# Kernel optimization log

Hardware: AMD Instinct MI355X
Metric: run time of the kernel (lower is better)

Reference implementation:

```python
import jax, jax.numpy as jnp
import numpy as np

SEQ = 110          # input_size1 = sample_width*2
HALF = SEQ // 2    # 55
N_EMBD = 102       # n_chrom + 2
HEAD = 192

def _cross_half_mask():
    # attention allowed only between the two halves (same-half blocks masked)
    idx = jnp.arange(SEQ)
    same_half = (idx[:, None] < HALF) == (idx[None, :] < HALF)
    return same_half  # True where attention is DISALLOWED

def setup_inputs() -> dict:
    key = jax.random.key(0)
    k1, k2, k3, k4 = jax.random.split(key, 4)
    B = 8192
    x = jax.random.normal(k1, (B, SEQ, N_EMBD), dtype=jnp.float32)
    Wq = jax.random.normal(k2, (N_EMBD, HEAD), dtype=jnp.float32) * (N_EMBD ** -0.5)
    Wk = jax.random.normal(k3, (N_EMBD, HEAD), dtype=jnp.float32) * (N_EMBD ** -0.5)
    Wv = jax.random.normal(k4, (N_EMBD, HEAD), dtype=jnp.float32) * (N_EMBD ** -0.5)
    return {"x": x, "Wq": Wq, "Wk": Wk, "Wv": Wv}

def reference(x, Wq, Wk, Wv):
    # q,k,v: [B, S, H]
    q = x @ Wq
    k = x @ Wk
    v = x @ Wv
    scale = HEAD ** -0.5
    scores = jnp.einsum('bsh,bth->bst', q, k) * scale  # [B, S, S]
    mask = _cross_half_mask()                           # [S, S] True = masked
    scores = jnp.where(mask, -jnp.inf, scores)
    attn = jax.nn.softmax(scores, axis=-1)
    # dropout is identity at inference (p=0.15 at train)
    out = jnp.einsum('bst,bth->bsh', attn, v)           # [B, S, H]
    return out
```

## Files before the change

kernel.cpp:

```cpp
#include <hip/hip_runtime.h>
#include <hip/hip_bf16.h>

#define SEQ   110
#define HALFS 55
#define EMB   102
#define HEAD  192

typedef short bf16x8 __attribute__((ext_vector_type(8)));
typedef float f32x4  __attribute__((ext_vector_type(4)));

#define XS    104
#define XTILE (64 * XS)
#define PS    72
#define MTS   128
#define MTROWS 112
#define MT_SHORTS (MTROWS * MTS)
#define WES   128

__device__ __forceinline__ short f2bf(float f) {
    unsigned u = __float_as_uint(f);
    unsigned r = u + 0x7fffu + ((u >> 16) & 1u);
    return (short)(r >> 16);
}
__device__ __forceinline__ unsigned pk2(float a, float b) {
    return ((unsigned)(unsigned short)f2bf(b) << 16) | (unsigned short)f2bf(a);
}

__global__ void prep(const float* __restrict__ Wq, const float* __restrict__ Wk,
                     const float* __restrict__ Wv, short* __restrict__ ws) {
    int flat = blockIdx.x * 256 + threadIdx.x;
    if (flat < MT_SHORTS) {
        int i = flat >> 7, j = flat & 127;
        float v = 0.0f;
        if (i < EMB && j < EMB) {
            const float4* q4 = (const float4*)(Wq + j * HEAD);
            const float4* k4 = (const float4*)(Wk + i * HEAD);
            float s = 0.0f;
            #pragma unroll 4
            for (int h4 = 0; h4 < HEAD / 4; ++h4) {
                float4 a = q4[h4], b = k4[h4];
                s += a.x * b.x + a.y * b.y + a.z * b.z + a.w * b.w;
            }
            v = s * 0.07216878364870322f;
        }
        ws[flat] = f2bf(v);
    } else if (flat < MT_SHORTS + HEAD * WES) {
        int idx = flat - MT_SHORTS;
        int h = idx >> 7, e = idx & 127;
        float v = (e < EMB) ? Wv[e * HEAD + h] : 0.0f;
        ws[flat] = f2bf(v);
    }
}

__global__ __launch_bounds__(512, 2)
void attn_head(const float* __restrict__ x, const short* __restrict__ ws,
               float* __restrict__ out, int B) {
    const int tid  = threadIdx.x;
    const int w8   = tid >> 6;
    const int h    = w8 >> 2;
    const int w4   = w8 & 3;
    const int lane = tid & 63;
    const int g    = lane >> 4;
    const int r    = lane & 15;

    __shared__ __attribute__((aligned(16))) short u[4 * XTILE];
    __shared__ __attribute__((aligned(16))) short P_lds[2][64 * PS];

    short* xh = u + h * XTILE;
    short* xo = u + (h ^ 1) * XTILE;
    short* yh = u + (2 + h) * XTILE;
    short* Ph = P_lds[h];

    const short* Mt  = ws;
    const short* WvT = ws + MT_SHORTS;

    bf16x8 wvf[3][4];
    #pragma unroll
    for (int mi = 0; mi < 3; ++mi) {
        const int hrow = 16 * (w4 + 4 * mi) + r;
        #pragma unroll
        for (int kk = 0; kk < 4; ++kk)
            wvf[mi][kk] = *(const bf16x8*)(WvT + hrow * WES + 32 * kk + 8 * g);
    }

    {
        unsigned long long* z = (unsigned long long*)u;
        if (tid < 468) z[(tid < 234 ? 1430 : 2860) + tid] = 0ull;
        if (tid < 110)
            *(unsigned*)(u + (tid & 1) * XTILE + (tid >> 1) * XS + 102) = 0u;
    }

    unsigned xv[11];
    auto loadx = [&](int batch) {
        const float2* xb2 = (const float2*)(x + (size_t)batch * (SEQ * EMB));
        #pragma unroll
        for (int it = 0; it < 11; ++it) {
            int idx = tid + it * 512;
            if (idx < 5610) { float2 v = xb2[idx]; xv[it] = pk2(v.x, v.y); }
        }
    };
    auto stagex = [&]() {
        #pragma unroll
        for (int it = 0; it < 11; ++it) {
            int idx = tid + it * 512;
            if (idx < 5610) {
                int row  = (int)(((unsigned)idx * 82242u) >> 22);
                int ec   = idx - 51 * row;
                int tile = row >= HALFS;
                int lr   = row - HALFS * tile;
                *(unsigned*)(u + tile * XTILE + lr * XS + 2 * ec) = xv[it];
            }
        }
    };

    loadx(blockIdx.x);
    const int stride = (int)gridDim.x;

    bf16x8 ax[4][4];
    bf16x8 zz = {};
    const int src0 = ((g & 1) << 5) + r;
    const int src1 = src0 + 16;
    const bool hi  = (g >> 1) != 0;

    #pragma unroll 1
    for (int p = blockIdx.x; p < B; p += stride) {
        stagex();
        __syncthreads();

        bf16x8 am[2][4];
        #pragma unroll
        for (int mi2 = 0; mi2 < 2; ++mi2) {
            const int mt = w4 + 4 * mi2;
            #pragma unroll
            for (int kk = 0; kk < 4; ++kk)
                am[mi2][kk] = (mt < 7) ? *(const bf16x8*)(Mt + (16 * mt + r) * MTS + 32 * kk + 8 * g) : zz;
        }

        #pragma unroll
        for (int stl = 0; stl < 4; ++stl) {
            const short* xb = xh + (16 * stl + r) * XS;
            bf16x8 bx[4];
            #pragma unroll
            for (int kk = 0; kk < 3; ++kk) bx[kk] = *(const bf16x8*)(xb + 32 * kk + 8 * g);
            bx[3] = zz;
            if (g == 0) bx[3] = *(const bf16x8*)(xb + 96);
            #pragma unroll
            for (int mi2 = 0; mi2 < 2; ++mi2) {
                const int mt = w4 + 4 * mi2;
                if (mt < 7) {
                    f32x4 acc = {0.f, 0.f, 0.f, 0.f};
                    #pragma unroll
                    for (int kk = 0; kk < 4; ++kk)
                        acc = __builtin_amdgcn_mfma_f32_16x16x32_bf16(am[mi2][kk], bx[kk], acc, 0, 0, 0);
                    if (mt < 6 || g < 2) {
                        uint2 t2; t2.x = pk2(acc[0], acc[1]); t2.y = pk2(acc[2], acc[3]);
                        *(uint2*)(yh + (16 * stl + r) * XS + 16 * mt + 4 * g) = t2;
                    }
                }
            }
        }

        #pragma unroll
        for (int mt = 0; mt < 4; ++mt) {
            const short* xb = xo + (16 * mt + r) * XS;
            #pragma unroll
            for (int kk = 0; kk < 3; ++kk) ax[mt][kk] = *(const bf16x8*)(xb + 32 * kk + 8 * g);
            ax[mt][3] = zz;
            if (g == 0) ax[mt][3] = *(const bf16x8*)(xb + 96);
        }

        unsigned vpk[4][3][2];
        #pragma unroll
        for (int st = 0; st < 4; ++st) {
            #pragma unroll
            for (int mi = 0; mi < 3; ++mi) {
                f32x4 acc = {0.f, 0.f, 0.f, 0.f};
                #pragma unroll
                for (int kk = 0; kk < 4; ++kk)
                    acc = __builtin_amdgcn_mfma_f32_16x16x32_bf16(ax[st][kk], wvf[mi][kk], acc, 0, 0, 0);
                vpk[st][mi][0] = pk2(acc[0], acc[1]);
                vpk[st][mi][1] = pk2(acc[2], acc[3]);
            }
        }
        bf16x8 va[3][2];
        #pragma unroll
        for (int mi = 0; mi < 3; ++mi) {
            unsigned e00 = (unsigned)__shfl((int)vpk[0][mi][0], src0), e01 = (unsigned)__shfl((int)vpk[0][mi][1], src0);
            unsigned e02 = (unsigned)__shfl((int)vpk[0][mi][0], src1), e03 = (unsigned)__shfl((int)vpk[0][mi][1], src1);
            unsigned f00 = (unsigned)__shfl((int)vpk[1][mi][0], src0), f01 = (unsigned)__shfl((int)vpk[1][mi][1], src0);
            unsigned f02 = (unsigned)__shfl((int)vpk[1][mi][0], src1), f03 = (unsigned)__shfl((int)vpk[1][mi][1], src1);
            uint4 u0;
            u0.x = hi ? f00 : e00; u0.y = hi ? f01 : e01; u0.z = hi ? f02 : e02; u0.w = hi ? f03 : e03;
            unsigned e10 = (unsigned)__shfl((int)vpk[2][mi][0], src0), e11 = (unsigned)__shfl((int)vpk[2][mi][1], src0);
            unsigned e12 = (unsigned)__shfl((int)vpk[2][mi][0], src1), e13 = (unsigned)__shfl((int)vpk[2][mi][1], src1);
            unsigned f10 = (unsigned)__shfl((int)vpk[3][mi][0], src0), f11 = (unsigned)__shfl((int)vpk[3][mi][1], src0);
            unsigned f12 = (unsigned)__shfl((int)vpk[3][mi][0], src1), f13 = (unsigned)__shfl((int)vpk[3][mi][1], src1);
            uint4 u1;
            u1.x = hi ? f10 : e10; u1.y = hi ? f11 : e11; u1.z = hi ? f12 : e12; u1.w = hi ? f13 : e13;
            __builtin_memcpy(&va[mi][0], &u0, 16);
            __builtin_memcpy(&va[mi][1], &u1, 16);
        }

        __syncthreads();

        if (p + stride < B) loadx(p + stride);

        {
            const short* yb = yh + (16 * w4 + r) * XS;
            bf16x8 by[4];
            #pragma unroll
            for (int kk = 0; kk < 3; ++kk) by[kk] = *(const bf16x8*)(yb + 32 * kk + 8 * g);
            by[3] = zz;
            if (g == 0) by[3] = *(const bf16x8*)(yb + 96);

            float sc[4][4];
            #pragma unroll
            for (int mt = 0; mt < 4; ++mt) {
                f32x4 acc = {0.f, 0.f, 0.f, 0.f};
                #pragma unroll
                for (int kk = 0; kk < 4; ++kk)
                    acc = __builtin_amdgcn_mfma_f32_16x16x32_bf16(ax[mt][kk], by[kk], acc, 0, 0, 0);
                #pragma unroll
                for (int j = 0; j < 4; ++j) sc[mt][j] = acc[j];
            }
            #pragma unroll
            for (int j = 0; j < 4; ++j)
                if (48 + 4 * g + j >= HALFS) sc[3][j] = -1e30f;

            float mx = -1e30f;
            #pragma unroll
            for (int mt = 0; mt < 4; ++mt) {
                #pragma unroll
                for (int j = 0; j < 4; ++j) mx = fmaxf(mx, sc[mt][j]);
            }
            mx = fmaxf(mx, __shfl_xor(mx, 16));
            mx = fmaxf(mx, __shfl_xor(mx, 32));
            float pr[4][4];
            float sum = 0.f;
            #pragma unroll
            for (int mt = 0; mt < 4; ++mt) {
                #pragma unroll
                for (int j = 0; j < 4; ++j) { pr[mt][j] = __expf(sc[mt][j] - mx); sum += pr[mt][j]; }
            }
            sum += __shfl_xor(sum, 16);
            sum += __shfl_xor(sum, 32);
            float rs = 1.0f / sum;

            #pragma unroll
            for (int mt = 0; mt < 4; ++mt) {
                uint2 t2;
                t2.x = pk2(pr[mt][0] * rs, pr[mt][1] * rs);
                t2.y = pk2(pr[mt][2] * rs, pr[mt][3] * rs);
                *(uint2*)(Ph + (16 * w4 + r) * PS + 16 * mt + 4 * g) = t2;
            }
        }
        __syncthreads();

        const size_t obase = (size_t)p * (SEQ * HEAD) + (size_t)(h * HALFS) * HEAD;
        #pragma unroll
        for (int c = 0; c < 4; ++c) {
            const short* pb = Ph + (16 * c + r) * PS + 8 * g;
            bf16x8 bp0 = *(const bf16x8*)(pb);
            bf16x8 bp1 = *(const bf16x8*)(pb + 32);
            const int srow  = 16 * c + r;
            const bool valid = srow < HALFS;
            float* orow = out + obase + (size_t)srow * HEAD;
            #pragma unroll
            for (int mi = 0; mi < 3; ++mi) {
                f32x4 acc = {0.f, 0.f, 0.f, 0.f};
                acc = __builtin_amdgcn_mfma_f32_16x16x32_bf16(va[mi][0], bp0, acc, 0, 0, 0);
                acc = __builtin_amdgcn_mfma_f32_16x16x32_bf16(va[mi][1], bp1, acc, 0, 0, 0);
                if (valid) {
                    float4 st4; st4.x = acc[0]; st4.y = acc[1]; st4.z = acc[2]; st4.w = acc[3];
                    *(float4*)(orow + 16 * (w4 + 4 * mi) + 4 * g) = st4;
                }
            }
        }
        __syncthreads();
    }
}

extern "C" void kernel_launch(void* const* d_in, const int* in_sizes, int n_in,
                              void* d_out, int out_size, void* d_ws, size_t ws_size,
                              hipStream_t stream) {
    const float* x  = (const float*)d_in[0];
    const float* Wq = (const float*)d_in[1];
    const float* Wk = (const float*)d_in[2];
    const float* Wv = (const float*)d_in[3];
    short* ws = (short*)d_ws;
    int B = in_sizes[0] / (SEQ * EMB);
    int prep_elems = MT_SHORTS + HEAD * WES;
    prep<<<(prep_elems + 255) / 256, 256, 0, stream>>>(Wq, Wk, Wv, ws);
    attn_head<<<512, 512, 0, stream>>>(x, ws, (float*)d_out, B);
}
```

Measured before the change: 323.7 us.

## Process two batches per loop iteration with double-buffered LDS and float4 loads

Restructures the persistent loop so each block handles two batch elements per iteration, with separate LDS tiles for each. Global loads of the next batches are issued early and staged into LDS after the score phase, overlapping memory traffic with compute and cutting barriers per batch. It also switches global reads to float4, reuses the Y buffer for P, and reloads the x operands from LDS instead of keeping them in registers. In exchange the LDS footprint roughly doubles and more prefetch registers are held, which may lower occupancy under the 2-blocks launch bound.

```diff
diff --git a/kernel.cpp b/kernel.cpp
--- a/kernel.cpp
+++ b/kernel.cpp
@@ -11,7 +11,6 @@
 
 #define XS    104
 #define XTILE (64 * XS)
-#define PS    72
 #define MTS   128
 #define MTROWS 112
 #define MT_SHORTS (MTROWS * MTS)
@@ -52,6 +51,183 @@
     }
 }
 
+#define LOADX(batch, v0, v1) do { \
+    const float4* xb4_ = (const float4*)(x + (size_t)(batch) * (SEQ * EMB)); \
+    _Pragma("unroll") \
+    for (int it_ = 0; it_ < 6; ++it_) { \
+        int i4_ = tid + it_ * 512; \
+        if (i4_ < 2805) { float4 v_ = xb4_[i4_]; v0[it_] = pk2(v_.x, v_.y); v1[it_] = pk2(v_.z, v_.w); } \
+    } \
+} while (0)
+
+#define STAGEX(base, v0, v1) do { \
+    _Pragma("unroll") \
+    for (int it_ = 0; it_ < 6; ++it_) { \
+        int i4_ = tid + it_ * 512; \
+        if (i4_ < 2805) { \
+            int fc_  = i4_ * 4; \
+            int row_ = (int)(((unsigned long long)fc_ * 41121ull) >> 22); \
+            int e_   = fc_ - row_ * EMB; \
+            int tile_ = row_ >= HALFS; \
+            int lr_   = row_ - HALFS * tile_; \
+            int ba_   = (base) + tile_ * XTILE + lr_ * XS + e_; \
+            if (e_ == 100) { \
+                int rowb_  = row_ + 1; \
+                int tileb_ = rowb_ >= HALFS; \
+                int lrb_   = rowb_ - HALFS * tileb_; \
+                *(unsigned*)(u + ba_) = v0[it_]; \
+                *(unsigned*)(u + (base) + tileb_ * XTILE + lrb_ * XS) = v1[it_]; \
+            } else { \
+                uint2 t2_; t2_.x = v0[it_]; t2_.y = v1[it_]; \
+                *(uint2*)(u + ba_) = t2_; \
+            } \
+        } \
+    } \
+} while (0)
+
+#define YGEMM(xh_, yh_) do { \
+    _Pragma("unroll") \
+    for (int stl = 0; stl < 4; ++stl) { \
+        const short* xb_ = (xh_) + (16 * stl + r) * XS; \
+        bf16x8 bx_[4]; \
+        _Pragma("unroll") \
+        for (int kk = 0; kk < 3; ++kk) bx_[kk] = *(const bf16x8*)(xb_ + 32 * kk + 8 * g); \
+        bx_[3] = zz; \
+        if (g == 0) bx_[3] = *(const bf16x8*)(xb_ + 96); \
+        _Pragma("unroll") \
+        for (int mi2 = 0; mi2 < 2; ++mi2) { \
+            const int mt = w4 + 4 * mi2; \
+            if (mt < 7) { \
+                f32x4 acc = {0.f, 0.f, 0.f, 0.f}; \
+                _Pragma("unroll") \
+                for (int kk = 0; kk < 4; ++kk) \
+                    acc = __builtin_amdgcn_mfma_f32_16x16x32_bf16(am[mi2][kk], bx_[kk], acc, 0, 0, 0); \
+                if (mt < 6 || g < 2) { \
+                    uint2 t2_; t2_.x = pk2(acc[0], acc[1]); t2_.y = pk2(acc[2], acc[3]); \
+                    *(uint2*)((yh_) + (16 * stl + r) * XS + 16 * mt + 4 * g) = t2_; \
+                } \
+            } \
+        } \
+    } \
+} while (0)
+
+#define VGEMM(xo_, va_) do { \
+    unsigned vpk_[4][3][2]; \
+    _Pragma("unroll") \
+    for (int st = 0; st < 4; ++st) { \
+        const short* xb_ = (xo_) + (16 * st + r) * XS; \
+        bf16x8 axm_[4]; \
+        _Pragma("unroll") \
+        for (int kk = 0; kk < 3; ++kk) axm_[kk] = *(const bf16x8*)(xb_ + 32 * kk + 8 * g); \
+        axm_[3] = zz; \
+        if (g == 0) axm_[3] = *(const bf16x8*)(xb_ + 96); \
+        _Pragma("unroll") \
+        for (int mi = 0; mi < 3; ++mi) { \
+            f32x4 acc = {0.f, 0.f, 0.f, 0.f}; \
+            _Pragma("unroll") \
+            for (int kk = 0; kk < 4; ++kk) \
+                acc = __builtin_amdgcn_mfma_f32_16x16x32_bf16(axm_[kk], wvf[mi][kk], acc, 0, 0, 0); \
+            vpk_[st][mi][0] = pk2(acc[0], acc[1]); \
+            vpk_[st][mi][1] = pk2(acc[2], acc[3]); \
+        } \
+    } \
+    _Pragma("unroll") \
+    for (int mi = 0; mi < 3; ++mi) { \
+        unsigned e00 = (unsigned)__shfl((int)vpk_[0][mi][0], src0), e01 = (unsigned)__shfl((int)vpk_[0][mi][1], src0); \
+        unsigned e02 = (unsigned)__shfl((int)vpk_[0][mi][0], src1), e03 = (unsigned)__shfl((int)vpk_[0][mi][1], src1); \
+        unsigned f00 = (unsigned)__shfl((int)vpk_[1][mi][0], src0), f01 = (unsigned)__shfl((int)vpk_[1][mi][1], src0); \
+        unsigned f02 = (unsigned)__shfl((int)vpk_[1][mi][0], src1), f03 = (unsigned)__shfl((int)vpk_[1][mi][1], src1); \
+        uint4 u0_; \
+        u0_.x = hi ? f00 : e00; u0_.y = hi ? f01 : e01; u0_.z = hi ? f02 : e02; u0_.w = hi ? f03 : e03; \
+        unsigned e10 = (unsigned)__shfl((int)vpk_[2][mi][0], src0), e11 = (unsigned)__shfl((int)vpk_[2][mi][1], src0); \
+        unsigned e12 = (unsigned)__shfl((int)vpk_[2][mi][0], src1), e13 = (unsigned)__shfl((int)vpk_[2][mi][1], src1); \
+        unsigned f10 = (unsigned)__shfl((int)vpk_[3][mi][0], src0), f11 = (unsigned)__shfl((int)vpk_[3][mi][1], src0); \
+        unsigned f12 = (unsigned)__shfl((int)vpk_[3][mi][0], src1), f13 = (unsigned)__shfl((int)vpk_[3][mi][1], src1); \
+        uint4 u1_; \
+        u1_.x = hi ? f10 : e10; u1_.y = hi ? f11 : e11; u1_.z = hi ? f12 : e12; u1_.w = hi ? f13 : e13; \
+        __builtin_memcpy(&va_[mi][0], &u0_, 16); \
+        __builtin_memcpy(&va_[mi][1], &u1_, 16); \
+    } \
+} while (0)
+
+#define SCORES_P(xo_, yh_) do { \
+    bf16x8 by_[4]; \
+    { \
+        const short* yb_ = (yh_) + (16 * w4 + r) * XS; \
+        _Pragma("unroll") \
+        for (int kk = 0; kk < 3; ++kk) by_[kk] = *(const bf16x8*)(yb_ + 32 * kk + 8 * g); \
+        by_[3] = zz; \
+        if (g == 0) by_[3] = *(const bf16x8*)(yb_ + 96); \
+    } \
+    float sc_[4][4]; \
+    _Pragma("unroll") \
+    for (int mt = 0; mt < 4; ++mt) { \
+        const short* xb_ = (xo_) + (16 * mt + r) * XS; \
+        bf16x8 axm_[4]; \
+        _Pragma("unroll") \
+        for (int kk = 0; kk < 3; ++kk) axm_[kk] = *(const bf16x8*)(xb_ + 32 * kk + 8 * g); \
+        axm_[3] = zz; \
+        if (g == 0) axm_[3] = *(const bf16x8*)(xb_ + 96); \
+        f32x4 acc = {0.f, 0.f, 0.f, 0.f}; \
+        _Pragma("unroll") \
+        for (int kk = 0; kk < 4; ++kk) \
+            acc = __builtin_amdgcn_mfma_f32_16x16x32_bf16(axm_[kk], by_[kk], acc, 0, 0, 0); \
+        _Pragma("unroll") \
+        for (int j = 0; j < 4; ++j) sc_[mt][j] = acc[j]; \
+    } \
+    _Pragma("unroll") \
+    for (int j = 0; j < 4; ++j) \
+        if (48 + 4 * g + j >= HALFS) sc_[3][j] = -1e30f; \
+    float mx_ = -1e30f; \
+    _Pragma("unroll") \
+    for (int mt = 0; mt < 4; ++mt) { \
+        _Pragma("unroll") \
+        for (int j = 0; j < 4; ++j) mx_ = fmaxf(mx_, sc_[mt][j]); \
+    } \
+    mx_ = fmaxf(mx_, __shfl_xor(mx_, 16)); \
+    mx_ = fmaxf(mx_, __shfl_xor(mx_, 32)); \
+    float pr_[4][4]; \
+    float sum_ = 0.f; \
+    _Pragma("unroll") \
+    for (int mt = 0; mt < 4; ++mt) { \
+        _Pragma("unroll") \
+        for (int j = 0; j < 4; ++j) { pr_[mt][j] = __expf(sc_[mt][j] - mx_); sum_ += pr_[mt][j]; } \
+    } \
+    sum_ += __shfl_xor(sum_, 16); \
+    sum_ += __shfl_xor(sum_, 32); \
+    float rs_ = 1.0f / sum_; \
+    _Pragma("unroll") \
+    for (int mt = 0; mt < 4; ++mt) { \
+        uint2 t2_; \
+        t2_.x = pk2(pr_[mt][0] * rs_, pr_[mt][1] * rs_); \
+        t2_.y = pk2(pr_[mt][2] * rs_, pr_[mt][3] * rs_); \
+        *(uint2*)((yh_) + (16 * w4 + r) * XS + 16 * mt + 4 * g) = t2_; \
+    } \
+} while (0)
+
+#define PVOUT(yh_, va_, pbatch) do { \
+    const size_t obase_ = (size_t)(pbatch) * (SEQ * HEAD) + (size_t)(h * HALFS) * HEAD; \
+    _Pragma("unroll") \
+    for (int c = 0; c < 4; ++c) { \
+        const short* pb_ = (yh_) + (16 * c + r) * XS + 8 * g; \
+        bf16x8 bp0_ = *(const bf16x8*)(pb_); \
+        bf16x8 bp1_ = *(const bf16x8*)(pb_ + 32); \
+        const int srow_ = 16 * c + r; \
+        const bool valid_ = srow_ < HALFS; \
+        float* orow_ = out + obase_ + (size_t)srow_ * HEAD; \
+        _Pragma("unroll") \
+        for (int mi = 0; mi < 3; ++mi) { \
+            f32x4 acc = {0.f, 0.f, 0.f, 0.f}; \
+            acc = __builtin_amdgcn_mfma_f32_16x16x32_bf16(va_[mi][0], bp0_, acc, 0, 0, 0); \
+            acc = __builtin_amdgcn_mfma_f32_16x16x32_bf16(va_[mi][1], bp1_, acc, 0, 0, 0); \
+            if (valid_) { \
+                float4 st4_; st4_.x = acc[0]; st4_.y = acc[1]; st4_.z = acc[2]; st4_.w = acc[3]; \
+                *(float4*)(orow_ + 16 * (w4 + 4 * mi) + 4 * g) = st4_; \
+            } \
+        } \
+    } \
+} while (0)
+
 __global__ __launch_bounds__(512, 2)
 void attn_head(const float* __restrict__ x, const short* __restrict__ ws,
                float* __restrict__ out, int B) {
@@ -63,13 +239,14 @@
     const int g    = lane >> 4;
     const int r    = lane & 15;
 
-    __shared__ __attribute__((aligned(16))) short u[4 * XTILE];
-    __shared__ __attribute__((aligned(16))) short P_lds[2][64 * PS];
-
-    short* xh = u + h * XTILE;
-    short* xo = u + (h ^ 1) * XTILE;
-    short* yh = u + (2 + h) * XTILE;
-    short* Ph = P_lds[h];
+    __shared__ __attribute__((aligned(16))) short u[8 * XTILE];
+
+    short* xhA = u + h * XTILE;
+    short* xoA = u + (h ^ 1) * XTILE;
+    short* xhB = u + (2 + h) * XTILE;
+    short* xoB = u + (2 + (h ^ 1)) * XTILE;
+    short* yhA = u + (4 + h) * XTILE;
+    short* yhB = u + (6 + h) * XTILE;
 
     const short* Mt  = ws;
     const short* WvT = ws + MT_SHORTS;
@@ -85,47 +262,48 @@
 
     {
         unsigned long long* z = (unsigned long long*)u;
-        if (tid < 468) z[(tid < 234 ? 1430 : 2860) + tid] = 0ull;
-        if (tid < 110)
-            *(unsigned*)(u + (tid & 1) * XTILE + (tid >> 1) * XS + 102) = 0u;
-    }
-
-    unsigned xv[11];
-    auto loadx = [&](int batch) {
-        const float2* xb2 = (const float2*)(x + (size_t)batch * (SEQ * EMB));
         #pragma unroll
-        for (int it = 0; it < 11; ++it) {
-            int idx = tid + it * 512;
-            if (idx < 5610) { float2 v = xb2[idx]; xv[it] = pk2(v.x, v.y); }
-        }
-    };
-    auto stagex = [&]() {
-        #pragma unroll
-        for (int it = 0; it < 11; ++it) {
-            int idx = tid + it * 512;
-            if (idx < 5610) {
-                int row  = (int)(((unsigned)idx * 82242u) >> 22);
-                int ec   = idx - 51 * row;
-                int tile = row >= HALFS;
-                int lr   = row - HALFS * tile;
-                *(unsigned*)(u + tile * XTILE + lr * XS + 2 * ec) = xv[it];
+        for (int i0 = 0; i0 < 2; ++i0) {
+            int ii = tid + i0 * 512;
+            if (ii < 936) {
+                int tt = ii / 234;
+                int o  = ii - tt * 234;
+                z[tt * 1664 + 1430 + o] = 0ull;
             }
         }
-    };
-
-    loadx(blockIdx.x);
-    const int stride = (int)gridDim.x;
-
-    bf16x8 ax[4][4];
+        if (tid < 220) {
+            int tt  = tid / 55;
+            int row = tid - tt * 55;
+            *(unsigned*)(u + tt * XTILE + row * XS + 102) = 0u;
+        }
+    }
+
+    const int gsz    = (int)gridDim.x;
+    const int stride2 = 2 * gsz;
+    unsigned xvA0[6], xvA1[6], xvB0[6], xvB1[6];
+
+    LOADX((int)blockIdx.x, xvA0, xvA1);
+    STAGEX(0, xvA0, xvA1);
+    if ((int)blockIdx.x + gsz < B) {
+        LOADX((int)blockIdx.x + gsz, xvB0, xvB1);
+        STAGEX(2 * XTILE, xvB0, xvB1);
+    }
+
     bf16x8 zz = {};
     const int src0 = ((g & 1) << 5) + r;
     const int src1 = src0 + 16;
     const bool hi  = (g >> 1) != 0;
 
     #pragma unroll 1
-    for (int p = blockIdx.x; p < B; p += stride) {
-        stagex();
+    for (int p = blockIdx.x; p < B; p += stride2) {
+        const int pB   = p + gsz;
+        const bool hasB = pB < B;
+        const int pnA  = p + stride2;
+        const int pnB  = pB + stride2;
+
         __syncthreads();
+
+        if (pnA < B) LOADX(pnA, xvA0, xvA1);
 
         bf16x8 am[2][4];
         #pragma unroll
@@ -136,147 +314,27 @@
                 am[mi2][kk] = (mt < 7) ? *(const bf16x8*)(Mt + (16 * mt + r) * MTS + 32 * kk + 8 * g) : zz;
         }
 
-        #pragma unroll
-        for (int stl = 0; stl < 4; ++stl) {
-            const short* xb = xh + (16 * stl + r) * XS;
-            bf16x8 bx[4];
-            #pragma unroll
-            for (int kk = 0; kk < 3; ++kk) bx[kk] = *(const bf16x8*)(xb + 32 * kk + 8 * g);
-            bx[3] = zz;
-            if (g == 0) bx[3] = *(const bf16x8*)(xb + 96);
-            #pragma unroll
-            for (int mi2 = 0; mi2 < 2; ++mi2) {
-                const int mt = w4 + 4 * mi2;
-                if (mt < 7) {
-                    f32x4 acc = {0.f, 0.f, 0.f, 0.f};
-                    #pragma unroll
-                    for (int kk = 0; kk < 4; ++kk)
-                        acc = __builtin_amdgcn_mfma_f32_16x16x32_bf16(am[mi2][kk], bx[kk], acc, 0, 0, 0);
-                    if (mt < 6 || g < 2) {
-                        uint2 t2; t2.x = pk2(acc[0], acc[1]); t2.y = pk2(acc[2], acc[3]);
-                        *(uint2*)(yh + (16 * stl + r) * XS + 16 * mt + 4 * g) = t2;
-                    }
-                }
-            }
-        }
-
-        #pragma unroll
-        for (int mt = 0; mt < 4; ++mt) {
-            const short* xb = xo + (16 * mt + r) * XS;
-            #pragma unroll
-            for (int kk = 0; kk < 3; ++kk) ax[mt][kk] = *(const bf16x8*)(xb + 32 * kk + 8 * g);
-            ax[mt][3] = zz;
-            if (g == 0) ax[mt][3] = *(const bf16x8*)(xb + 96);
-        }
-
-        unsigned vpk[4][3][2];
-        #pragma unroll
-        for (int st = 0; st < 4; ++st) {
-            #pragma unroll
-            for (int mi = 0; mi < 3; ++mi) {
-                f32x4 acc = {0.f, 0.f, 0.f, 0.f};
-                #pragma unroll
-                for (int kk = 0; kk < 4; ++kk)
-                    acc = __builtin_amdgcn_mfma_f32_16x16x32_bf16(ax[st][kk], wvf[mi][kk], acc, 0, 0, 0);
-                vpk[st][mi][0] = pk2(acc[0], acc[1]);
-                vpk[st][mi][1] = pk2(acc[2], acc[3]);
-            }
-        }
-        bf16x8 va[3][2];
-        #pragma unroll
-        for (int mi = 0; mi < 3; ++mi) {
-            unsigned e00 = (unsigned)__shfl((int)vpk[0][mi][0], src0), e01 = (unsigned)__shfl((int)vpk[0][mi][1], src0);
-            unsigned e02 = (unsigned)__shfl((int)vpk[0][mi][0], src1), e03 = (unsigned)__shfl((int)vpk[0][mi][1], src1);
-            unsigned f00 = (unsigned)__shfl((int)vpk[1][mi][0], src0), f01 = (unsigned)__shfl((int)vpk[1][mi][1], src0);
-            unsigned f02 = (unsigned)__shfl((int)vpk[1][mi][0], src1), f03 = (unsigned)__shfl((int)vpk[1][mi][1], src1);
-            uint4 u0;
-            u0.x = hi ? f00 : e00; u0.y = hi ? f01 : e01; u0.z = hi ? f02 : e02; u0.w = hi ? f03 : e03;
-            unsigned e10 = (unsigned)__shfl((int)vpk[2][mi][0], src0), e11 = (unsigned)__shfl((int)vpk[2][mi][1], src0);
-            unsigned e12 = (unsigned)__shfl((int)vpk[2][mi][0], src1), e13 = (unsigned)__shfl((int)vpk[2][mi][1], src1);
-            unsigned f10 = (unsigned)__shfl((int)vpk[3][mi][0], src0), f11 = (unsigned)__shfl((int)vpk[3][mi][1], src0);
-            unsigned f12 = (unsigned)__shfl((int)vpk[3][mi][0], src1), f13 = (unsigned)__shfl((int)vpk[3][mi][1], src1);
-            uint4 u1;
-            u1.x = hi ? f10 : e10; u1.y = hi ? f11 : e11; u1.z = hi ? f12 : e12; u1.w = hi ? f13 : e13;
-            __builtin_memcpy(&va[mi][0], &u0, 16);
-            __builtin_memcpy(&va[mi][1], &u1, 16);
-        }
+        YGEMM(xhA, yhA);
+        if (hasB) YGEMM(xhB, yhB);
+
+        bf16x8 vaA[3][2], vaB[3][2];
+        VGEMM(xoA, vaA);
+        if (hasB) VGEMM(xoB, vaB);
 
         __syncthreads();
 
-        if (p + stride < B) loadx(p + stride);
-
-        {
-            const short* yb = yh + (16 * w4 + r) * XS;
-            bf16x8 by[4];
-            #pragma unroll
-            for (int kk = 0; kk < 3; ++kk) by[kk] = *(const bf16x8*)(yb + 32 * kk + 8 * g);
-            by[3] = zz;
-            if (g == 0) by[3] = *(const bf16x8*)(yb + 96);
-
-            float sc[4][4];
-            #pragma unroll
-            for (int mt = 0; mt < 4; ++mt) {
-                f32x4 acc = {0.f, 0.f, 0.f, 0.f};
-                #pragma unroll
-                for (int kk = 0; kk < 4; ++kk)
-                    acc = __builtin_amdgcn_mfma_f32_16x16x32_bf16(ax[mt][kk], by[kk], acc, 0, 0, 0);
-                #pragma unroll
-                for (int j = 0; j < 4; ++j) sc[mt][j] = acc[j];
-            }
-            #pragma unroll
-            for (int j = 0; j < 4; ++j)
-                if (48 + 4 * g + j >= HALFS) sc[3][j] = -1e30f;
-
-            float mx = -1e30f;
-            #pragma unroll
-            for (int mt = 0; mt < 4; ++mt) {
-                #pragma unroll
-                for (int j = 0; j < 4; ++j) mx = fmaxf(mx, sc[mt][j]);
-            }
-            mx = fmaxf(mx, __shfl_xor(mx, 16));
-            mx = fmaxf(mx, __shfl_xor(mx, 32));
-            float pr[4][4];
-            float sum = 0.f;
-            #pragma unroll
-            for (int mt = 0; mt < 4; ++mt) {
-                #pragma unroll
-                for (int j = 0; j < 4; ++j) { pr[mt][j] = __expf(sc[mt][j] - mx); sum += pr[mt][j]; }
-            }
-            sum += __shfl_xor(sum, 16);
-            sum += __shfl_xor(sum, 32);
-            float rs = 1.0f / sum;
-
-            #pragma unroll
-            for (int mt = 0; mt < 4; ++mt) {
-                uint2 t2;
-                t2.x = pk2(pr[mt][0] * rs, pr[mt][1] * rs);
-                t2.y = pk2(pr[mt][2] * rs, pr[mt][3] * rs);
-                *(uint2*)(Ph + (16 * w4 + r) * PS + 16 * mt + 4 * g) = t2;
-            }
-        }
+        SCORES_P(xoA, yhA);
+        if (hasB) SCORES_P(xoB, yhB);
+
+        if (hasB && pnB < B) LOADX(pnB, xvB0, xvB1);
+
         __syncthreads();
 
-        const size_t obase = (size_t)p * (SEQ * HEAD) + (size_t)(h * HALFS) * HEAD;
-        #pragma unroll
-        for (int c = 0; c < 4; ++c) {
-            const short* pb = Ph + (16 * c + r) * PS + 8 * g;
-            bf16x8 bp0 = *(const bf16x8*)(pb);
-            bf16x8 bp1 = *(const bf16x8*)(pb + 32);
-            const int srow  = 16 * c + r;
-            const bool valid = srow < HALFS;
-            float* orow = out + obase + (size_t)srow * HEAD;
-            #pragma unroll
-            for (int mi = 0; mi < 3; ++mi) {
-                f32x4 acc = {0.f, 0.f, 0.f, 0.f};
-                acc = __builtin_amdgcn_mfma_f32_16x16x32_bf16(va[mi][0], bp0, acc, 0, 0, 0);
-                acc = __builtin_amdgcn_mfma_f32_16x16x32_bf16(va[mi][1], bp1, acc, 0, 0, 0);
-                if (valid) {
-                    float4 st4; st4.x = acc[0]; st4.y = acc[1]; st4.z = acc[2]; st4.w = acc[3];
-                    *(float4*)(orow + 16 * (w4 + 4 * mi) + 4 * g) = st4;
-                }
-            }
-        }
-        __syncthreads();
+        if (pnA < B) STAGEX(0, xvA0, xvA1);
+        if (pnB < B) STAGEX(2 * XTILE, xvB0, xvB1);
+
+        PVOUT(yhA, vaA, p);
+        if (hasB) PVOUT(yhB, vaB, pB);
     }
 }
 
```

After: 339.1 us. 4.8% more time.
